# Performance work log

Hardware: AMD Instinct MI355X
Metric: run time of the kernel (lower is better)

Reference implementation:

```python
import jax, jax.numpy as jnp
import numpy as np

N, D, F = 4096, 4096, 16384  # tokens, d_model, d_ff


def setup_inputs() -> dict:
    key = jax.random.key(0)
    ks = jax.random.split(key, 8)
    q_in = jax.random.randint(ks[0], (N, D), -127, 128, dtype=jnp.int32)
    in_scale = jax.random.uniform(ks[1], (N,), dtype=jnp.float32) * 0.01 + 1e-4
    w1_q = jax.random.randint(ks[2], (F, D), -127, 128, dtype=jnp.int32)
    w1_scale = jax.random.uniform(ks[3], (F,), dtype=jnp.float32) * 0.01 + 1e-4
    b1 = jax.random.normal(ks[4], (F,), dtype=jnp.float32) * 0.02
    w2_q = jax.random.randint(ks[5], (D, F), -127, 128, dtype=jnp.int32)
    w2_scale = jax.random.uniform(ks[6], (D,), dtype=jnp.float32) * 0.01 + 1e-4
    b2 = jax.random.normal(ks[7], (D,), dtype=jnp.float32) * 0.02
    return {"q_in": q_in, "in_scale": in_scale, "w1_q": w1_q, "w1_scale": w1_scale,
            "b1": b1, "w2_q": w2_q, "w2_scale": w2_scale, "b2": b2}


def _dynamic_quant(x):
    # per-token abs-max dynamic quantization to int8 range
    s = jnp.max(jnp.abs(x), axis=-1, keepdims=True) / 127.0
    s = jnp.maximum(s, 1e-8)
    q = jnp.clip(jnp.round(x / s), -128.0, 127.0)
    return q, s


def reference(q_in, in_scale, w1_q, w1_scale, b1, w2_q, w2_scale, b2):
    y1 = jnp.einsum('nd,fd->nf', q_in.astype(jnp.float32), w1_q.astype(jnp.float32))
    y1 = y1 * in_scale[:, None] * w1_scale[None, :] + b1[None, :]
    # fused gelu + dynamic re-quantization epilogue
    a = jax.nn.gelu(y1, approximate=False)
    q2, s2 = _dynamic_quant(a)
    # fc2
    y2 = jnp.einsum('nf,df->nd', q2, w2_q.astype(jnp.float32))
    y2 = y2 * s2 * w2_scale[None, :] + b2[None, :]
    return y2
```

## Files before the change

kernel.cpp:

```cpp
#include <hip/hip_runtime.h>
#include <hip/hip_bf16.h>
#include <cstdint>
#include <math.h>

#define TOKENS 4096
#define DMODEL 4096
#define DFF    16384

typedef __attribute__((ext_vector_type(4))) int i32x4;
typedef __attribute__((address_space(1))) unsigned int glb_u32;
typedef __attribute__((address_space(3))) unsigned int lds_u32;

__global__ void pack_i8_kernel(const int* __restrict__ src, unsigned* __restrict__ dst, long n4) {
    long i = (long)blockIdx.x * blockDim.x + threadIdx.x;
    const long stride = (long)gridDim.x * blockDim.x;
    for (; i < n4; i += stride) {
        const int4 v = ((const int4*)src)[i];
        unsigned p = (unsigned(v.x) & 255u) | ((unsigned(v.y) & 255u) << 8) |
                     ((unsigned(v.z) & 255u) << 16) | ((unsigned(v.w) & 255u) << 24);
        dst[i] = p;
    }
}

__global__ void zero_u32_kernel(unsigned* __restrict__ p, int n) {
    int i = blockIdx.x * blockDim.x + threadIdx.x;
    if (i < n) p[i] = 0u;
}

template <int EPI>
__global__ __launch_bounds__(512)
void gemm_i8_kernel(const int8_t* __restrict__ A,
                    const int8_t* __restrict__ B,
                    const int Nout, const int K,
                    const float* __restrict__ scaleA,
                    const float* __restrict__ scaleB,
                    const float* __restrict__ bias,
                    unsigned* __restrict__ rowmax,
                    __hip_bfloat16* __restrict__ aout,
                    float* __restrict__ out)
{
    __shared__ int8_t As[2][256 * 128];
    __shared__ int8_t Bs[2][256 * 128];

    const int tid  = threadIdx.x;
    const int lane = tid & 63;
    const int w    = tid >> 6;
    const int wm   = w >> 2;
    const int wn   = w & 3;
    const int l15  = lane & 15, l4 = lane >> 4;

    const int gx  = gridDim.x;
    const int nwg = gx * gridDim.y;
    int wg = blockIdx.y * gx + blockIdx.x;
    wg = (wg & 7) * (nwg >> 3) + (wg >> 3);
    const int col0 = (wg % gx) * 256;
    const int row0 = (wg / gx) * 256;

    const int nt = K >> 7;

    const int g16 = ((lane & 7) ^ (lane >> 3)) << 4;

    const int rbA = (((wm << 7) + l15) << 7);
    const int rbB = (((wn << 6) + l15) << 7);
    const int c0  = (l4 ^ (l15 & 7)) << 4;

    i32x4 fAlo[4], fAhi[4], fB[4];
    i32x4 acc[8][4] = {};

#define STAGE_UNIT(P, p0q, LDSARR, bufi, t, u)                                        \
    {                                                                                 \
        const int8_t* src_ = (P) + (size_t)((p0q) + (u) * 64 + (w << 3) +             \
                             (lane >> 3)) * K + ((t) << 7) + g16;                     \
        int8_t* dst_ = &LDSARR[bufi][(u) * 8192 + (w << 10)];                         \
        __builtin_amdgcn_global_load_lds((glb_u32*)src_, (lds_u32*)dst_, 16, 0, 0);   \
    }

#define MFMA_Q(FA, MB)                                                                \
    {                                                                                 \
        __builtin_amdgcn_s_setprio(1);                                                \
        _Pragma("unroll")                                                             \
        for (int m_ = 0; m_ < 4; ++m_)                                                \
            _Pragma("unroll")                                                         \
            for (int n_ = 0; n_ < 4; ++n_)                                            \
                acc[(MB) + m_][n_] = __builtin_amdgcn_mfma_i32_16x16x64_i8(           \
                    FA[m_], fB[n_], acc[(MB) + m_][n_], 0, 0, 0);                     \
        __builtin_amdgcn_s_setprio(0);                                                \
    }

#pragma unroll
    for (int u = 0; u < 4; ++u) STAGE_UNIT(B, col0, Bs, 0, 0, u);
#pragma unroll
    for (int u = 0; u < 4; ++u) STAGE_UNIT(A, row0, As, 0, 0, u);
    asm volatile("s_waitcnt vmcnt(0)" ::: "memory");
    __builtin_amdgcn_s_barrier();

    for (int t = 0; t < nt; ++t) {
        const int buf  = t & 1;
        const int nbuf = buf ^ 1;
        const int tn   = (t + 1 < nt) ? (t + 1) : (nt - 1);

#pragma unroll
        for (int m = 0; m < 4; ++m)
            fAlo[m] = *(const i32x4*)(&As[buf][rbA + m * 2048 + c0]);
#pragma unroll
        for (int n = 0; n < 4; ++n)
            fB[n] = *(const i32x4*)(&Bs[buf][rbB + n * 2048 + c0]);
        STAGE_UNIT(B, col0, Bs, nbuf, tn, 0);
        STAGE_UNIT(B, col0, Bs, nbuf, tn, 1);
        __builtin_amdgcn_sched_barrier(0);
        __builtin_amdgcn_s_barrier();
        asm volatile("s_waitcnt lgkmcnt(0)" ::: "memory");
        __builtin_amdgcn_sched_barrier(0);
        MFMA_Q(fAlo, 0);
        asm volatile("s_waitcnt vmcnt(2)" ::: "memory");
        __builtin_amdgcn_s_barrier();

#pragma unroll
        for (int m = 0; m < 4; ++m)
            fAhi[m] = *(const i32x4*)(&As[buf][rbA + (m + 4) * 2048 + c0]);
        STAGE_UNIT(B, col0, Bs, nbuf, tn, 2);
        STAGE_UNIT(B, col0, Bs, nbuf, tn, 3);
        __builtin_amdgcn_sched_barrier(0);
        __builtin_amdgcn_s_barrier();
        asm volatile("s_waitcnt lgkmcnt(0)" ::: "memory");
        __builtin_amdgcn_sched_barrier(0);
        MFMA_Q(fAhi, 4);
        __builtin_amdgcn_s_barrier();

#pragma unroll
        for (int m = 0; m < 4; ++m)
            fAlo[m] = *(const i32x4*)(&As[buf][rbA + m * 2048 + (c0 ^ 64)]);
#pragma unroll
        for (int n = 0; n < 4; ++n)
            fB[n] = *(const i32x4*)(&Bs[buf][rbB + n * 2048 + (c0 ^ 64)]);
        STAGE_UNIT(A, row0, As, nbuf, tn, 0);
        STAGE_UNIT(A, row0, As, nbuf, tn, 2);
        __builtin_amdgcn_sched_barrier(0);
        __builtin_amdgcn_s_barrier();
        asm volatile("s_waitcnt lgkmcnt(0)" ::: "memory");
        __builtin_amdgcn_sched_barrier(0);
        MFMA_Q(fAlo, 0);
        __builtin_amdgcn_s_barrier();

#pragma unroll
        for (int m = 0; m < 4; ++m)
            fAhi[m] = *(const i32x4*)(&As[buf][rbA + (m + 4) * 2048 + (c0 ^ 64)]);
        STAGE_UNIT(A, row0, As, nbuf, tn, 1);
        STAGE_UNIT(A, row0, As, nbuf, tn, 3);
        __builtin_amdgcn_sched_barrier(0);
        __builtin_amdgcn_s_barrier();
        asm volatile("s_waitcnt lgkmcnt(0)" ::: "memory");
        __builtin_amdgcn_sched_barrier(0);
        MFMA_Q(fAhi, 4);
        asm volatile("s_waitcnt vmcnt(2)" ::: "memory");
        __builtin_amdgcn_s_barrier();
    }
#undef STAGE_UNIT
#undef MFMA_Q

    if (EPI == 1) {
#pragma unroll
        for (int m = 0; m < 8; ++m) {
#pragma unroll
            for (int reg = 0; reg < 4; ++reg) {
                const int grow = row0 + (wm << 7) + m * 16 + l4 * 4 + reg;
                const float sa = scaleA[grow];
                float vmax = 0.0f;
#pragma unroll
                for (int n = 0; n < 4; ++n) {
                    const int gcol = col0 + (wn << 6) + n * 16 + l15;
                    const float y = (float)acc[m][n][reg] * sa * scaleB[gcol] + bias[gcol];
                    const float gl = 0.5f * y * (1.0f + erff(y * 0.70710678118654752f));
                    aout[(size_t)grow * DFF + gcol] = __float2bfloat16(gl);
                    vmax = fmaxf(vmax, fabsf(gl));
                }
#pragma unroll
                for (int off = 1; off < 16; off <<= 1)
                    vmax = fmaxf(vmax, __shfl_xor(vmax, off));
                if (l15 == 0) atomicMax(&rowmax[grow], __float_as_uint(vmax));
            }
        }
    } else {
#pragma unroll
        for (int m = 0; m < 8; ++m) {
#pragma unroll
            for (int reg = 0; reg < 4; ++reg) {
                const int grow = row0 + (wm << 7) + m * 16 + l4 * 4 + reg;
                const float s2 = fmaxf(__uint_as_float(rowmax[grow]) * (1.0f / 127.0f), 1e-8f);
#pragma unroll
                for (int n = 0; n < 4; ++n) {
                    const int gcol = col0 + (wn << 6) + n * 16 + l15;
                    out[(size_t)grow * Nout + gcol] =
                        (float)acc[m][n][reg] * s2 * scaleB[gcol] + bias[gcol];
                }
            }
        }
    }
}

__global__ void quant_kernel(const unsigned short* __restrict__ a,
                             const unsigned* __restrict__ rowmax,
                             int8_t* __restrict__ q2)
{
    const size_t nvec = (size_t)TOKENS * DFF / 8;
    size_t i = (size_t)blockIdx.x * blockDim.x + threadIdx.x;
    const size_t stride = (size_t)gridDim.x * blockDim.x;
    for (; i < nvec; i += stride) {
        const size_t e0 = i * 8;
        const int n = (int)(e0 >> 14);
        const float s2 = fmaxf(__uint_as_float(rowmax[n]) * (1.0f / 127.0f), 1e-8f);
        const float inv = 1.0f / s2;
        const uint4 v = *(const uint4*)(a + e0);
        const unsigned words[4] = {v.x, v.y, v.z, v.w};
        int qi[8];
#pragma unroll
        for (int j = 0; j < 4; ++j) {
            const float f0 = __uint_as_float((words[j] & 0xffffu) << 16);
            const float f1 = __uint_as_float(words[j] & 0xffff0000u);
            qi[2 * j]     = (int)fminf(fmaxf(rintf(f0 * inv), -128.0f), 127.0f);
            qi[2 * j + 1] = (int)fminf(fmaxf(rintf(f1 * inv), -128.0f), 127.0f);
        }
        const unsigned p0 = (unsigned(qi[0]) & 255u) | ((unsigned(qi[1]) & 255u) << 8) |
                            ((unsigned(qi[2]) & 255u) << 16) | ((unsigned(qi[3]) & 255u) << 24);
        const unsigned p1 = (unsigned(qi[4]) & 255u) | ((unsigned(qi[5]) & 255u) << 8) |
                            ((unsigned(qi[6]) & 255u) << 16) | ((unsigned(qi[7]) & 255u) << 24);
        ((uint2*)q2)[i] = make_uint2(p0, p1);
    }
}

extern "C" void kernel_launch(void* const* d_in, const int* in_sizes, int n_in,
                              void* d_out, int out_size, void* d_ws, size_t ws_size,
                              hipStream_t stream) {
    const int*   q_in     = (const int*)d_in[0];
    const float* in_scale = (const float*)d_in[1];
    const int*   w1_q     = (const int*)d_in[2];
    const float* w1_scale = (const float*)d_in[3];
    const float* b1       = (const float*)d_in[4];
    const int*   w2_q     = (const int*)d_in[5];
    const float* w2_scale = (const float*)d_in[6];
    const float* b2       = (const float*)d_in[7];
    float* out = (float*)d_out;

    char* ws = (char*)d_ws;
    int8_t* A1 = (int8_t*)(ws);
    int8_t* W1 = (int8_t*)(ws + (size_t)16  * 1048576);
    int8_t* W2 = (int8_t*)(ws + (size_t)80  * 1048576);
    int8_t* Q2 = (int8_t*)(ws + (size_t)144 * 1048576);
    unsigned short* ABUF = (unsigned short*)(ws + (size_t)208 * 1048576);
    unsigned* ROWMAX = (unsigned*)(ws + (size_t)336 * 1048576);

    zero_u32_kernel<<<dim3(16), dim3(256), 0, stream>>>(ROWMAX, TOKENS);
    pack_i8_kernel<<<dim3(1024), dim3(256), 0, stream>>>(q_in, (unsigned*)A1, (long)TOKENS * DMODEL / 4);
    pack_i8_kernel<<<dim3(4096), dim3(256), 0, stream>>>(w1_q, (unsigned*)W1, (long)DFF * DMODEL / 4);
    pack_i8_kernel<<<dim3(4096), dim3(256), 0, stream>>>(w2_q, (unsigned*)W2, (long)DMODEL * DFF / 4);

    gemm_i8_kernel<1><<<dim3(DFF / 256, TOKENS / 256), dim3(512), 0, stream>>>(
        A1, W1, DFF, DMODEL, in_scale, w1_scale, b1, ROWMAX,
        (__hip_bfloat16*)ABUF, nullptr);

    quant_kernel<<<dim3(4096), dim3(256), 0, stream>>>(ABUF, ROWMAX, Q2);

    gemm_i8_kernel<2><<<dim3(DMODEL / 256, TOKENS / 256), dim3(512), 0, stream>>>(
        Q2, W2, DMODEL, DFF, nullptr, w2_scale, b2, ROWMAX,
        nullptr, out);
}
```

Measured before the change: 965.3 us.

## Switch int8 GEMM to four-stage K=64 pipeline with XCD-aware tile mapping

Cuts the K tile from 128 to 64 and moves from a double-buffered LDS ring to a four-buffer ring with three tiles prefetched ahead, waiting on vmcnt(8) so more global loads stay in flight. The LDS swizzle and staging addresses are reworked for the 64-byte rows. Workgroup-to-tile mapping becomes a 2x4 XCD grid with small strips per XCD to improve L2 locality. The cost is more loop iterations and barriers per K, plus mapping that assumes grid dimensions divisible by the chosen strip sizes.

New measurement: 978.6 us. No clear change (+1.4%).

```diff
diff --git a/kernel.cpp b/kernel.cpp
--- a/kernel.cpp
+++ b/kernel.cpp
@@ -39,8 +39,8 @@
                     __hip_bfloat16* __restrict__ aout,
                     float* __restrict__ out)
 {
-    __shared__ int8_t As[2][256 * 128];
-    __shared__ int8_t Bs[2][256 * 128];
+    __shared__ int8_t As[4][256 * 64];
+    __shared__ int8_t Bs[4][256 * 64];
 
     const int tid  = threadIdx.x;
     const int lane = tid & 63;
@@ -49,33 +49,37 @@
     const int wn   = w & 3;
     const int l15  = lane & 15, l4 = lane >> 4;
 
-    const int gx  = gridDim.x;
-    const int nwg = gx * gridDim.y;
-    int wg = blockIdx.y * gx + blockIdx.x;
-    wg = (wg & 7) * (nwg >> 3) + (wg >> 3);
-    const int col0 = (wg % gx) * 256;
-    const int row0 = (wg / gx) * 256;
-
-    const int nt = K >> 7;
-
-    const int g16 = ((lane & 7) ^ (lane >> 3)) << 4;
-
-    const int rbA = (((wm << 7) + l15) << 7);
-    const int rbB = (((wn << 6) + l15) << 7);
-    const int c0  = (l4 ^ (l15 & 7)) << 4;
-
-    i32x4 fAlo[4], fAhi[4], fB[4];
+    const int gx = gridDim.x, gy = gridDim.y;
+    const int wg  = blockIdx.y * gx + blockIdx.x;
+    const int xcd = wg & 7;
+    const int idx = wg >> 3;
+    const int xr = xcd >> 2, xc = xcd & 3;
+    const int strip = idx >> 5;
+    const int row_t = xr * (gy >> 1) + ((idx & 31) >> 2);
+    const int col_t = xc * (gx >> 2) + strip * 4 + (idx & 3);
+    const int row0 = row_t * 256;
+    const int col0 = col_t * 256;
+
+    const int nt = K >> 6;
+
+    const int g16 = ((lane & 3) ^ ((lane >> 3) & 3)) << 4;
+
+    const int rbA = ((wm << 7) + l15) << 6;
+    const int rbB = ((wn << 6) + l15) << 6;
+    const int c0  = (l4 ^ ((l15 >> 1) & 3)) << 4;
+
+    i32x4 fA[4], fB[4];
     i32x4 acc[8][4] = {};
 
 #define STAGE_UNIT(P, p0q, LDSARR, bufi, t, u)                                        \
     {                                                                                 \
-        const int8_t* src_ = (P) + (size_t)((p0q) + (u) * 64 + (w << 3) +             \
-                             (lane >> 3)) * K + ((t) << 7) + g16;                     \
+        const int8_t* src_ = (P) + (size_t)((p0q) + (u) * 128 + (w << 4) +            \
+                             (lane >> 2)) * K + ((t) << 6) + g16;                     \
         int8_t* dst_ = &LDSARR[bufi][(u) * 8192 + (w << 10)];                         \
         __builtin_amdgcn_global_load_lds((glb_u32*)src_, (lds_u32*)dst_, 16, 0, 0);   \
     }
 
-#define MFMA_Q(FA, MB)                                                                \
+#define MFMA_Q(MB)                                                                    \
     {                                                                                 \
         __builtin_amdgcn_s_setprio(1);                                                \
         _Pragma("unroll")                                                             \
@@ -83,76 +87,51 @@
             _Pragma("unroll")                                                         \
             for (int n_ = 0; n_ < 4; ++n_)                                            \
                 acc[(MB) + m_][n_] = __builtin_amdgcn_mfma_i32_16x16x64_i8(           \
-                    FA[m_], fB[n_], acc[(MB) + m_][n_], 0, 0, 0);                     \
+                    fA[m_], fB[n_], acc[(MB) + m_][n_], 0, 0, 0);                     \
         __builtin_amdgcn_s_setprio(0);                                                \
     }
 
 #pragma unroll
-    for (int u = 0; u < 4; ++u) STAGE_UNIT(B, col0, Bs, 0, 0, u);
-#pragma unroll
-    for (int u = 0; u < 4; ++u) STAGE_UNIT(A, row0, As, 0, 0, u);
-    asm volatile("s_waitcnt vmcnt(0)" ::: "memory");
+    for (int tt = 0; tt < 3; ++tt) {
+        STAGE_UNIT(A, row0, As, tt, tt, 0);
+        STAGE_UNIT(A, row0, As, tt, tt, 1);
+        STAGE_UNIT(B, col0, Bs, tt, tt, 0);
+        STAGE_UNIT(B, col0, Bs, tt, tt, 1);
+    }
+    asm volatile("s_waitcnt vmcnt(8)" ::: "memory");
     __builtin_amdgcn_s_barrier();
 
     for (int t = 0; t < nt; ++t) {
-        const int buf  = t & 1;
-        const int nbuf = buf ^ 1;
-        const int tn   = (t + 1 < nt) ? (t + 1) : (nt - 1);
+        const int buf = t & 3;
+        const int tn  = (t + 3 < nt) ? (t + 3) : (nt - 1);
+        const int nbuf = tn & 3;
 
 #pragma unroll
         for (int m = 0; m < 4; ++m)
-            fAlo[m] = *(const i32x4*)(&As[buf][rbA + m * 2048 + c0]);
+            fA[m] = *(const i32x4*)(&As[buf][rbA + m * 1024 + c0]);
 #pragma unroll
         for (int n = 0; n < 4; ++n)
-            fB[n] = *(const i32x4*)(&Bs[buf][rbB + n * 2048 + c0]);
+            fB[n] = *(const i32x4*)(&Bs[buf][rbB + n * 1024 + c0]);
+        STAGE_UNIT(A, row0, As, nbuf, tn, 0);
+        STAGE_UNIT(A, row0, As, nbuf, tn, 1);
+        __builtin_amdgcn_sched_barrier(0);
+        __builtin_amdgcn_s_barrier();
+        asm volatile("s_waitcnt lgkmcnt(0)" ::: "memory");
+        __builtin_amdgcn_sched_barrier(0);
+        MFMA_Q(0);
+        __builtin_amdgcn_s_barrier();
+
+#pragma unroll
+        for (int m = 0; m < 4; ++m)
+            fA[m] = *(const i32x4*)(&As[buf][rbA + (m + 4) * 1024 + c0]);
         STAGE_UNIT(B, col0, Bs, nbuf, tn, 0);
         STAGE_UNIT(B, col0, Bs, nbuf, tn, 1);
         __builtin_amdgcn_sched_barrier(0);
         __builtin_amdgcn_s_barrier();
         asm volatile("s_waitcnt lgkmcnt(0)" ::: "memory");
         __builtin_amdgcn_sched_barrier(0);
-        MFMA_Q(fAlo, 0);
-        asm volatile("s_waitcnt vmcnt(2)" ::: "memory");
-        __builtin_amdgcn_s_barrier();
-
-#pragma unroll
-        for (int m = 0; m < 4; ++m)
-            fAhi[m] = *(const i32x4*)(&As[buf][rbA + (m + 4) * 2048 + c0]);
-        STAGE_UNIT(B, col0, Bs, nbuf, tn, 2);
-        STAGE_UNIT(B, col0, Bs, nbuf, tn, 3);
-        __builtin_amdgcn_sched_barrier(0);
-        __builtin_amdgcn_s_barrier();
-        asm volatile("s_waitcnt lgkmcnt(0)" ::: "memory");
-        __builtin_amdgcn_sched_barrier(0);
-        MFMA_Q(fAhi, 4);
-        __builtin_amdgcn_s_barrier();
-
-#pragma unroll
-        for (int m = 0; m < 4; ++m)
-            fAlo[m] = *(const i32x4*)(&As[buf][rbA + m * 2048 + (c0 ^ 64)]);
-#pragma unroll
-        for (int n = 0; n < 4; ++n)
-            fB[n] = *(const i32x4*)(&Bs[buf][rbB + n * 2048 + (c0 ^ 64)]);
-        STAGE_UNIT(A, row0, As, nbuf, tn, 0);
-        STAGE_UNIT(A, row0, As, nbuf, tn, 2);
-        __builtin_amdgcn_sched_barrier(0);
-        __builtin_amdgcn_s_barrier();
-        asm volatile("s_waitcnt lgkmcnt(0)" ::: "memory");
-        __builtin_amdgcn_sched_barrier(0);
-        MFMA_Q(fAlo, 0);
-        __builtin_amdgcn_s_barrier();
-
-#pragma unroll
-        for (int m = 0; m < 4; ++m)
-            fAhi[m] = *(const i32x4*)(&As[buf][rbA + (m + 4) * 2048 + (c0 ^ 64)]);
-        STAGE_UNIT(A, row0, As, nbuf, tn, 1);
-        STAGE_UNIT(A, row0, As, nbuf, tn, 3);
-        __builtin_amdgcn_sched_barrier(0);
-        __builtin_amdgcn_s_barrier();
-        asm volatile("s_waitcnt lgkmcnt(0)" ::: "memory");
-        __builtin_amdgcn_sched_barrier(0);
-        MFMA_Q(fAhi, 4);
-        asm volatile("s_waitcnt vmcnt(2)" ::: "memory");
+        MFMA_Q(4);
+        asm volatile("s_waitcnt vmcnt(8)" ::: "memory");
         __builtin_amdgcn_s_barrier();
     }
 #undef STAGE_UNIT
```
